# Optimization experiments

Hardware: AMD Instinct MI355X
Metric: run time of the kernel (lower is better)

## Reference

```python
import jax, jax.numpy as jnp
import numpy as np

L, C, H = 4, 512, 8
HD = C // H

def silu(x):
    return x * jax.nn.sigmoid(x)

def layernorm(x, g, b, eps=1e-5):
    m = x.mean(-1, keepdims=True)
    v = ((x - m) ** 2).mean(-1, keepdims=True)
    return (x - m) * jax.lax.rsqrt(v + eps) * g + b

def adaln(x, t, w, b):
    # x: (N,B,C), t: (B,C), w: (2C,C), b: (2C,)
    mod = silu(t) @ w.T + b
    scale, shift = jnp.split(mod, 2, axis=-1)
    return x * (1.0 + scale[None]) + shift[None]

def embed_rotary(x, pos):
    # x: (B,N,C), pos: (B,N,C,2) with [...,0]=cos, [...,1]=sin
    cos, sin = pos[..., 0], pos[..., 1]
    x2 = jnp.stack([-x[..., 1::2], x[..., 0::2]], axis=-1).reshape(x.shape)
    return x * cos + x2 * sin

def setup_inputs() -> dict:
    key = jax.random.key(0)
    ks = jax.random.split(key, 24)
    Nq, Nkv, B = 1024, 2048, 4
    query = jax.random.normal(ks[0], (Nq, B, C), jnp.float32)
    value = jax.random.normal(ks[1], (Nkv, B, C), jnp.float32)
    diff_ts = jax.random.normal(ks[2], (B, C), jnp.float32)
    # valid rotary codes: cos/sin of random angles
    aq = jax.random.uniform(ks[3], (B, Nq, C), jnp.float32, 0.0, 2 * np.pi)
    ak = jax.random.uniform(ks[4], (B, Nkv, C), jnp.float32, 0.0, 2 * np.pi)
    query_pos = jnp.stack([jnp.cos(aq), jnp.sin(aq)], axis=-1)
    value_pos = jnp.stack([jnp.cos(ak), jnp.sin(ak)], axis=-1)
    s = 0.02
    inp = dict(query=query, value=value, diff_ts=diff_ts,
               query_pos=query_pos, value_pos=value_pos,
               aw_attn=jax.random.normal(ks[5], (L, 2 * C, C)) * s,
               ab_attn=jax.random.normal(ks[6], (L, 2 * C)) * s,
               in_w=jax.random.normal(ks[7], (L, 3 * C, C)) * s,
               in_b=jnp.zeros((L, 3 * C)),
               out_w=jax.random.normal(ks[8], (L, C, C)) * s,
               out_b=jnp.zeros((L, C)),
               ln1_g=jnp.ones((L, C)), ln1_b=jnp.zeros((L, C)),
               aw_ffn=jax.random.normal(ks[9], (L, 2 * C, C)) * s,
               ab_ffn=jax.random.normal(ks[10], (L, 2 * C)) * s,
               w1=jax.random.normal(ks[11], (L, C, C)) * s,
               b1=jnp.zeros((L, C)),
               w2=jax.random.normal(ks[12], (L, C, C)) * s,
               b2=jnp.zeros((L, C)),
               ln2_g=jnp.ones((L, C)), ln2_b=jnp.zeros((L, C)))
    return inp

def _forward(query, value, diff_ts, query_pos, value_pos,
             aw_attn, ab_attn, in_w, in_b, out_w, out_b, ln1_g, ln1_b,
             aw_ffn, ab_ffn, w1, b1, w2, b2, ln2_g, ln2_b):
    Nq, B, _ = query.shape
    Nkv = value.shape[0]
    scaling = HD ** -0.5
    outputs = []
    q = query
    for i in range(L):
        # --- cross-attention layer ---
        aq = adaln(q, diff_ts, aw_attn[i], ab_attn[i])
        wq, wk, wv = jnp.split(in_w[i], 3, axis=0)
        bq, bk, bv = jnp.split(in_b[i], 3, axis=0)
        qp = (aq @ wq.T + bq) * scaling          # (Nq,B,C)
        kp = value @ wk.T + bk                    # (Nkv,B,C)
        vp = value @ wv.T + bv
        qb = embed_rotary(qp.transpose(1, 0, 2), query_pos)  # (B,Nq,C)
        kb = embed_rotary(kp.transpose(1, 0, 2), value_pos)  # (B,Nkv,C)
        vb = vp.transpose(1, 0, 2)
        qh = qb.reshape(B, Nq, H, HD).transpose(0, 2, 1, 3)   # (B,H,Nq,HD)
        kh = kb.reshape(B, Nkv, H, HD).transpose(0, 2, 1, 3)
        vh = vb.reshape(B, Nkv, H, HD).transpose(0, 2, 1, 3)
        scores = jnp.einsum('bhqd,bhkd->bhqk', qh, kh)
        attn = jax.nn.softmax(scores, axis=-1)
        o = jnp.einsum('bhqk,bhkd->bhqd', attn, vh)
        o = o.transpose(0, 2, 1, 3).reshape(B, Nq, C).transpose(1, 0, 2)  # (Nq,B,C)
        o = o @ out_w[i].T + out_b[i]
        q = layernorm(q + o, ln1_g[i], ln1_b[i])
        # --- feedforward layer (residual uses AdaLN-modulated x) ---
        xa = adaln(q, diff_ts, aw_ffn[i], ab_ffn[i])
        h = jax.nn.relu(xa @ w1[i].T + b1[i])
        h = h @ w2[i].T + b2[i]
        q = layernorm(xa + h, ln2_g[i], ln2_b[i])
        outputs.append(q)
    return jnp.stack(outputs)  # (L, Nq, B, C)

def reference(query, value, diff_ts, query_pos, value_pos,
              aw_attn, ab_attn, in_w, in_b, out_w, out_b, ln1_g, ln1_b,
              aw_ffn, ab_ffn, w1, b1, w2, b2, ln2_g, ln2_b):
    return _forward(query, value, diff_ts, query_pos, value_pos,
                    aw_attn, ab_attn, in_w, in_b, out_w, out_b, ln1_g, ln1_b,
                    aw_ffn, ab_ffn, w1, b1, w2, b2, ln2_g, ln2_b)
```

## Files before the change

kernel.cpp:

```cpp
#include <hip/hip_runtime.h>
#include <hip/hip_bf16.h>

typedef __hip_bfloat16 bf16;
typedef __attribute__((ext_vector_type(8))) short short8;
typedef __attribute__((ext_vector_type(4))) short s16x4;
typedef __attribute__((ext_vector_type(4))) float f32x4;

#define CDIM 512
#define BDIM 4
#define HDIM 8
#define HDQ  64
#define NQ   1024
#define NKV  2048
#define LAYERS 4
#define SPLIT 2

#if defined(__has_builtin)
#if __has_builtin(__builtin_amdgcn_global_load_lds)
#define USE_GLL 1
#endif
#endif

static __device__ __forceinline__ short f2s(float f) {
    bf16 h = __float2bfloat16(f);
    return *reinterpret_cast<short*>(&h);
}


__global__ __launch_bounds__(256) void convall_k(
    const float* __restrict__ s0, const float* __restrict__ s1,
    const float* __restrict__ s2, const float* __restrict__ s3,
    const float* __restrict__ s4,
    bf16* __restrict__ d0, bf16* __restrict__ d1, bf16* __restrict__ d2,
    bf16* __restrict__ d3, bf16* __restrict__ d4) {
    int gid = blockIdx.x * 256 + threadIdx.x;
    const float* src; bf16* dst; int off;
    if (gid < 1048576)      { src = s0; dst = d0; off = gid; }
    else if (gid < 1835008) { src = s1; dst = d1; off = gid - 1048576; }
    else if (gid < 2097152) { src = s2; dst = d2; off = gid - 1835008; }
    else if (gid < 2359296) { src = s3; dst = d3; off = gid - 2097152; }
    else                    { src = s4; dst = d4; off = gid - 2359296; }
    f32x4 v = *(const f32x4*)(src + (size_t)off * 4);
    s16x4 o;
    o[0] = f2s(v[0]); o[1] = f2s(v[1]); o[2] = f2s(v[2]); o[3] = f2s(v[3]);
    *(s16x4*)(dst + (size_t)off * 4) = o;
}

__global__ __launch_bounds__(256) void modall_k(const float* __restrict__ diff_ts,
    const float* __restrict__ aw_attn, const float* __restrict__ ab_attn,
    const float* __restrict__ aw_ffn,  const float* __restrict__ ab_ffn,
    float* __restrict__ mod) {
    int wv = blockIdx.x * 4 + (threadIdx.x >> 6);
    int lane = threadIdx.x & 63;
    int col  = wv & 1023;
    int b    = (wv >> 10) & 3;
    int kind = (wv >> 12) & 1;
    int l    = wv >> 13;
    const float* w = (kind ? aw_ffn : aw_attn) + ((size_t)l * 1024 + col) * CDIM + lane * 8;
    const float* tb = diff_ts + b * CDIM + lane * 8;
    f32x4 w0 = *(const f32x4*)w;
    f32x4 w1 = *(const f32x4*)(w + 4);
    f32x4 t0 = *(const f32x4*)tb;
    f32x4 t1 = *(const f32x4*)(tb + 4);
    #pragma unroll
    for (int j = 0; j < 4; ++j) {
        t0[j] = t0[j] / (1.f + __expf(-t0[j]));
        t1[j] = t1[j] / (1.f + __expf(-t1[j]));
    }
    f32x4 pp = w0 * t0 + w1 * t1;
    float acc = (pp[0] + pp[1]) + (pp[2] + pp[3]);
    #pragma unroll
    for (int off = 32; off; off >>= 1) acc += __shfl_xor(acc, off);
    if (lane == 0)
        mod[wv] = acc + (kind ? ab_ffn : ab_attn)[l * 1024 + col];
}

__global__ __launch_bounds__(256) void adaln_k(const float* __restrict__ x,
                                               const float* __restrict__ mod,
                                               bf16* __restrict__ outb) {
    int i = blockIdx.x * 256 + threadIdx.x;
    int c = i & 511;
    int b = (i >> 9) & 3;
    outb[i] = __float2bfloat16(x[i] * (1.f + mod[b * 1024 + c]) + mod[b * 1024 + 512 + c]);
}

__global__ __launch_bounds__(256) void ln_ad_k(const float* __restrict__ x,
                                               const float* __restrict__ res,
                                               const float* __restrict__ res2,
                                               const float* __restrict__ g,
                                               const float* __restrict__ bb,
                                               const float* __restrict__ mod,
                                               float* __restrict__ ln_f,
                                               float* __restrict__ ln_f2,
                                               float* __restrict__ ad_f,
                                               bf16* __restrict__ ad_b) {
    int row = blockIdx.x;
    int t = threadIdx.x;
    size_t base = (size_t)row * CDIM;
    float v0 = x[base + t] + res[base + t];
    float v1 = x[base + t + 256] + res[base + t + 256];
    if (res2) {
        v0 += res2[base + t];
        v1 += res2[base + t + 256];
    }
    float s1 = v0 + v1;
    float s2 = v0 * v0 + v1 * v1;
    #pragma unroll
    for (int off = 32; off; off >>= 1) {
        s1 += __shfl_xor(s1, off);
        s2 += __shfl_xor(s2, off);
    }
    __shared__ float a1[4], a2[4];
    int w = t >> 6;
    if ((t & 63) == 0) { a1[w] = s1; a2[w] = s2; }
    __syncthreads();
    s1 = a1[0] + a1[1] + a1[2] + a1[3];
    s2 = a2[0] + a2[1] + a2[2] + a2[3];
    float mean = s1 * (1.f / 512.f);
    float var = s2 * (1.f / 512.f) - mean * mean;
    float rs = rsqrtf(var + 1e-5f);
    float y0 = (v0 - mean) * rs * g[t] + bb[t];
    float y1 = (v1 - mean) * rs * g[t + 256] + bb[t + 256];
    if (ln_f)  { ln_f[base + t] = y0;  ln_f[base + t + 256] = y1; }
    if (ln_f2) { ln_f2[base + t] = y0; ln_f2[base + t + 256] = y1; }
    if (mod) {
        int b = row & 3;
        float o0 = y0 * (1.f + mod[b * 1024 + t]) + mod[b * 1024 + 512 + t];
        float o1 = y1 * (1.f + mod[b * 1024 + t + 256]) + mod[b * 1024 + 512 + t + 256];
        if (ad_f) { ad_f[base + t] = o0; ad_f[base + t + 256] = o1; }
        ad_b[base + t] = __float2bfloat16(o0);
        ad_b[base + t + 256] = __float2bfloat16(o1);
    }
}

template <int EPI, int WM, int NT, int KS, bool SWZ>
__global__ __launch_bounds__(256) void mgemm_k(
    const bf16* __restrict__ A, const bf16* __restrict__ Wt,
    const float* __restrict__ bias, void* __restrict__ out0v,
    void* __restrict__ out1v, int M, int N, int K,
    const float* __restrict__ pos, float scl, int Nseq) {
    __shared__ bf16 As[2][2][64 * 32];
    __shared__ bf16 Bs[2][2][64 * 32];
    int t = threadIdx.x;
    int w = t >> 6;
    int lane = t & 63;
    int l16 = lane & 15;
    int quad = lane >> 4;
    int wy = w >> 1, wx = w & 1;

    int bxi, byi, bzi;
    if (SWZ) {
        int nx = gridDim.x, ny = gridDim.y;
        int flat = (blockIdx.z * ny + blockIdx.y) * nx + blockIdx.x;
        int nwg = nx * ny * gridDim.z;
        int s = (flat & 7) * (nwg >> 3) + (flat >> 3);
        bxi = s % nx; int rest = s / nx; byi = rest % ny; bzi = rest / ny;
    } else {
        bxi = blockIdx.x; byi = blockIdx.y; bzi = blockIdx.z;
    }
    int bm = byi * 64;
    int bn = bxi * 64;

    int lr2 = lane >> 2;
    int lc4 = (lane & 3) ^ ((lane >> 3) & 3);

    int kbeg = 0, kend = K;
    if (KS == 2) { int half = K >> 1; kbeg = bzi * half; kend = kbeg + half; }

    f32x4 acc[WM][NT] = {};

    auto stage = [&](int buf, int k0) {
#if USE_GLL
        const bf16* sa = A + (size_t)(bm + w * 16 + lr2) * K + k0 + lc4 * 8;
        const bf16* sb = Wt + (size_t)(bn + w * 16 + lr2) * K + k0 + lc4 * 8;
        #pragma unroll
        for (int j = 0; j < 2; ++j) {
            __builtin_amdgcn_global_load_lds(
                (const unsigned int __attribute__((address_space(1)))*)(sa + j * 32),
                (unsigned int __attribute__((address_space(3)))*)(&As[buf][j][w * 512]),
                16, 0, 0);
            __builtin_amdgcn_global_load_lds(
                (const unsigned int __attribute__((address_space(1)))*)(sb + j * 32),
                (unsigned int __attribute__((address_space(3)))*)(&Bs[buf][j][w * 512]),
                16, 0, 0);
        }
#else
        for (int e = t; e < 512; e += 256) {
            int sub = e >> 8, c = e & 255;
            int row = c >> 2, c4 = c & 3;
            int srcc = c4 ^ ((row >> 1) & 3);
            *(uint4*)&As[buf][sub][row * 32 + c4 * 8] =
                *(const uint4*)(A + (size_t)(bm + row) * K + k0 + sub * 32 + srcc * 8);
            *(uint4*)&Bs[buf][sub][row * 32 + c4 * 8] =
                *(const uint4*)(Wt + (size_t)(bn + row) * K + k0 + sub * 32 + srcc * 8);
        }
#endif
    };

    stage(0, kbeg);
    __syncthreads();
    int cur = 0;
    int rchunk = (quad ^ ((l16 >> 1) & 3)) * 8;

    for (int k0 = kbeg; k0 < kend; k0 += 64) {
        if (k0 + 64 < kend) stage(cur ^ 1, k0 + 64);

        #pragma unroll
        for (int kk = 0; kk < 2; ++kk) {
            short8 af[WM], bfr[NT];
            #pragma unroll
            for (int mt = 0; mt < WM; ++mt)
                af[mt] = *(const short8*)
                    &As[cur][kk][((wy * WM + mt) * 16 + l16) * 32 + rchunk];
            #pragma unroll
            for (int nt = 0; nt < NT; ++nt)
                bfr[nt] = *(const short8*)
                    &Bs[cur][kk][((wx * NT + nt) * 16 + l16) * 32 + rchunk];
            #pragma unroll
            for (int mt = 0; mt < WM; ++mt)
                #pragma unroll
                for (int nt = 0; nt < NT; ++nt)
                    acc[mt][nt] = __builtin_amdgcn_mfma_f32_16x16x32_bf16(
                        af[mt], bfr[nt], acc[mt][nt], 0, 0, 0);
        }

        __syncthreads();
        cur ^= 1;
    }

    float* fout = (KS == 2 && bzi) ? (float*)out1v : (float*)out0v;
    #pragma unroll
    for (int nt = 0; nt < NT; ++nt) {
        int n = bn + (wx * NT + nt) * 16 + l16;
        float bnv = (EPI == 4 || (KS == 2 && bzi)) ? 0.f : bias[n];
        #pragma unroll
        for (int mt = 0; mt < WM; ++mt) {
            #pragma unroll
            for (int r = 0; r < 4; ++r) {
                int m = bm + (wy * WM + mt) * 16 + quad * 4 + r;
                float v = acc[mt][nt][r] + ((EPI == 4) ? bias[m] : bnv);
                if (EPI == 0) {
                    fout[(size_t)m * N + n] = v;
                } else if (EPI == 1) {
                    ((bf16*)out0v)[(size_t)m * N + n] = __float2bfloat16(fmaxf(v, 0.f));
                } else if (EPI == 4) {
                    int hh = m >> 6, dd = m & 63;
                    int bsel = n & 3, key = n >> 2;
                    ((bf16*)out0v)[((size_t)(bsel * HDIM + hh) * HDQ + dd) * NKV + key] =
                        __float2bfloat16(v);
                } else {
                    v *= scl;
                    int c = n;
                    int nseq = m >> 2, b = m & 3;
                    float part = __shfl_xor(v, 1);
                    const float* pp = pos + (((size_t)b * Nseq + nseq) * CDIM + c) * 2;
                    float cs = pp[0], sn = pp[1];
                    float o = (l16 & 1) ? (v * cs + part * sn) : (v * cs - part * sn);
                    bf16* op = (bf16*)out0v +
                               ((size_t)(b * HDIM + (c >> 6)) * Nseq + nseq) * HDQ + (c & 63);
                    *op = __float2bfloat16(o);
                }
            }
        }
    }
}

__global__ __launch_bounds__(256) void attn4_k(const bf16* __restrict__ qh,
                                               const bf16* __restrict__ kh,
                                               const bf16* __restrict__ vT,
                                               float* __restrict__ pl,
                                               float* __restrict__ pacc) {
    __shared__ short Kb[2][64 * 64];
    __shared__ short Vb[2][64 * 64];
    __shared__ short Ps[4][16 * 64];
    int t = threadIdx.x;
    int wave = t >> 6, lane = t & 63;
    int l16 = lane & 15, quad = lane >> 4;

    int b0 = blockIdx.x;
    int newid = (b0 & 7) * 128 + (b0 >> 3);
    int qtile = newid & 15;
    int grp = newid >> 4;
    int split = grp & 1;
    int bh = grp >> 1;
    int q0 = qtile * 64 + wave * 16;
    int kbase = split * (NKV / SPLIT);

    const bf16* qbase = qh + ((size_t)bh * NQ + q0) * HDQ;
    short8 aq0 = *(const short8*)(qbase + (size_t)l16 * HDQ + quad * 8);
    short8 aq1 = *(const short8*)(qbase + (size_t)l16 * HDQ + 32 + quad * 8);
    const bf16* kbh = kh + ((size_t)bh * NKV + kbase) * HDQ;
    const bf16* vbh = vT + (size_t)bh * HDQ * NKV + kbase;

    int r0 = wave * 16;
    int lr = lane >> 3;
    int swz_src = ((lane & 7) ^ lr) * 8;

    auto stage = [&](int buf, int kt) {
#if USE_GLL
        #pragma unroll
        for (int j = 0; j < 2; ++j) {
            int rr = r0 + j * 8;
            __builtin_amdgcn_global_load_lds(
                (const unsigned int __attribute__((address_space(1)))*)
                    (kbh + (size_t)(kt + rr + lr) * HDQ + swz_src),
                (unsigned int __attribute__((address_space(3)))*)&Kb[buf][rr * 64],
                16, 0, 0);
            __builtin_amdgcn_global_load_lds(
                (const unsigned int __attribute__((address_space(1)))*)
                    (vbh + (size_t)(rr + lr) * NKV + kt + swz_src),
                (unsigned int __attribute__((address_space(3)))*)&Vb[buf][rr * 64],
                16, 0, 0);
        }
#else
        #pragma unroll
        for (int j = 0; j < 2; ++j) {
            int rr = r0 + j * 8 + lr;
            int lc = lane & 7;
            *(short8*)&Kb[buf][rr * 64 + ((lc ^ (rr & 7)) * 8)] =
                *(const short8*)(kbh + (size_t)(kt + rr) * HDQ + lc * 8);
            *(short8*)&Vb[buf][rr * 64 + ((lc ^ (rr & 7)) * 8)] =
                *(const short8*)(vbh + (size_t)rr * NKV + kt + lc * 8);
        }
#endif
    };

    f32x4 accO[4] = {};
    float lsum[4] = {0.f, 0.f, 0.f, 0.f};

    stage(0, 0);
    __syncthreads();
    int cur = 0;
    int swz_m = l16 & 7;

    for (int kt = 0; kt < NKV / SPLIT; kt += 64) {
        if (kt + 64 < NKV / SPLIT) stage(cur ^ 1, kt + 64);

        f32x4 sc[4] = {};
        #pragma unroll
        for (int nt = 0; nt < 4; ++nt) {
            const short* kr = &Kb[cur][(nt * 16 + l16) * 64];
            short8 bk0 = *(const short8*)&kr[(quad ^ swz_m) * 8];
            short8 bk1 = *(const short8*)&kr[((quad + 4) ^ swz_m) * 8];
            sc[nt] = __builtin_amdgcn_mfma_f32_16x16x32_bf16(aq0, bk0, sc[nt], 0, 0, 0);
            sc[nt] = __builtin_amdgcn_mfma_f32_16x16x32_bf16(aq1, bk1, sc[nt], 0, 0, 0);
        }

        #pragma unroll
        for (int r = 0; r < 4; ++r) {
            float p0 = exp2f(sc[0][r]);
            float p1 = exp2f(sc[1][r]);
            float p2 = exp2f(sc[2][r]);
            float p3 = exp2f(sc[3][r]);
            lsum[r] += (p0 + p1) + (p2 + p3);
            int pr = quad * 4 + r;
            short* prow = &Ps[wave][pr * 64];
            int pm = pr & 7;
            int ch = l16 >> 3, kl = l16 & 7;
            prow[((ch ^ pm) << 3) + kl]       = f2s(p0);
            prow[(((ch + 2) ^ pm) << 3) + kl] = f2s(p1);
            prow[(((ch + 4) ^ pm) << 3) + kl] = f2s(p2);
            prow[(((ch + 6) ^ pm) << 3) + kl] = f2s(p3);
        }

        const short* prd = &Ps[wave][l16 * 64];
        short8 pa0 = *(const short8*)&prd[(quad ^ swz_m) * 8];
        short8 pa1 = *(const short8*)&prd[((quad + 4) ^ swz_m) * 8];
        #pragma unroll
        for (int nt = 0; nt < 4; ++nt) {
            const short* vr = &Vb[cur][(nt * 16 + l16) * 64];
            short8 bv0 = *(const short8*)&vr[(quad ^ swz_m) * 8];
            short8 bv1 = *(const short8*)&vr[((quad + 4) ^ swz_m) * 8];
            accO[nt] = __builtin_amdgcn_mfma_f32_16x16x32_bf16(pa0, bv0, accO[nt], 0, 0, 0);
            accO[nt] = __builtin_amdgcn_mfma_f32_16x16x32_bf16(pa1, bv1, accO[nt], 0, 0, 0);
        }

        __syncthreads();
        cur ^= 1;
    }

    #pragma unroll
    for (int r = 0; r < 4; ++r) {
        #pragma unroll
        for (int off = 1; off < 16; off <<= 1) lsum[r] += __shfl_xor(lsum[r], off);
    }

    size_t rowbase = ((size_t)split * 32 + bh) * NQ + q0;
    #pragma unroll
    for (int r = 0; r < 4; ++r) {
        size_t row = rowbase + quad * 4 + r;
        if (l16 == 0) pl[row] = lsum[r];
        #pragma unroll
        for (int nt = 0; nt < 4; ++nt)
            pacc[row * 64 + nt * 16 + l16] = accO[nt][r];
    }
}

__global__ __launch_bounds__(256) void attn_comb_k(const float* __restrict__ pl,
                                                   const float* __restrict__ pacc,
                                                   bf16* __restrict__ o) {
    int idx = blockIdx.x * 256 + threadIdx.x;
    int d = idx & 63;
    int row = idx >> 6;
    int q = row & (NQ - 1);
    int bh = row >> 10;
    const int S = 32 * NQ;
    float l = pl[row] + pl[S + row];
    float v = pacc[(size_t)row * 64 + d] + pacc[(size_t)(S + row) * 64 + d];
    int b = bh >> 3, h = bh & 7;
    o[((size_t)(q * BDIM + b)) * CDIM + h * HDQ + d] = __float2bfloat16(v / l);
}


extern "C" void kernel_launch(void* const* d_in, const int* in_sizes, int n_in,
                              void* d_out, int out_size, void* d_ws, size_t ws_size,
                              hipStream_t stream) {
    const float* query     = (const float*)d_in[0];
    const float* value     = (const float*)d_in[1];
    const float* diff_ts   = (const float*)d_in[2];
    const float* query_pos = (const float*)d_in[3];
    const float* value_pos = (const float*)d_in[4];
    const float* aw_attn   = (const float*)d_in[5];
    const float* ab_attn   = (const float*)d_in[6];
    const float* in_w      = (const float*)d_in[7];
    const float* in_b      = (const float*)d_in[8];
    const float* out_w     = (const float*)d_in[9];
    const float* out_b     = (const float*)d_in[10];
    const float* ln1_g     = (const float*)d_in[11];
    const float* ln1_b     = (const float*)d_in[12];
    const float* aw_ffn    = (const float*)d_in[13];
    const float* ab_ffn    = (const float*)d_in[14];
    const float* w1        = (const float*)d_in[15];
    const float* b1        = (const float*)d_in[16];
    const float* w2        = (const float*)d_in[17];
    const float* b2        = (const float*)d_in[18];
    const float* ln2_g     = (const float*)d_in[19];
    const float* ln2_b     = (const float*)d_in[20];
    float* out_f = (float*)d_out;

    float* ws      = (float*)d_ws;
    float* mod_ws  = ws + 2048;
    float* q_cur   = ws + 34816;
    float* buf_a   = q_cur + 2097152;
    float* buf_p   = buf_a + 2097152;
    bf16* a_bf     = (bf16*)(buf_p + 2097152);
    bf16* h_bf     = a_bf + 2097152;
    bf16* qh       = h_bf + 2097152;
    bf16* kh       = qh + 2097152;
    bf16* vt       = kh + 4194304;
    bf16* val_bf   = vt + 4194304;
    bf16* winb     = val_bf + 4194304;
    bf16* woutb    = winb + 3145728;
    bf16* w1b      = woutb + 1048576;
    bf16* w2b      = w1b + 1048576;
    float* buf_p2  = (float*)(w2b + 1048576);
    float* pacc    = buf_a;
    float* pl      = (float*)a_bf;

    const int MQ = NQ * BDIM;
    const int MKV = NKV * BDIM;
    const float scaling = 0.125f * 1.44269504f;

    modall_k<<<8192, 256, 0, stream>>>(diff_ts, aw_attn, ab_attn, aw_ffn, ab_ffn, mod_ws);
    convall_k<<<10240, 256, 0, stream>>>(value, in_w, out_w, w1, w2,
                                         val_bf, winb, woutb, w1b, w2b);
    adaln_k<<<(MQ * CDIM) / 256, 256, 0, stream>>>(query, mod_ws, a_bf);

    for (int i = 0; i < LAYERS; ++i) {
        const float* mod_ffn  = mod_ws + i * 8192 + 4096;
        const float* mod_attn_next = (i + 1 < LAYERS) ? (mod_ws + (i + 1) * 8192) : nullptr;
        const bf16* winb_i = winb + (size_t)i * 1536 * CDIM;
        const float* in_b_i = in_b + (size_t)i * 1536;
        const float* qsrc = (i == 0) ? query : q_cur;

        mgemm_k<2, 2, 2, 1, true><<<dim3(8, MQ / 64), 256, 0, stream>>>(
            a_bf, winb_i, in_b_i, qh, nullptr, MQ, 512, CDIM, query_pos, scaling, NQ);
        mgemm_k<2, 2, 2, 1, true><<<dim3(8, MKV / 64), 256, 0, stream>>>(
            val_bf, winb_i + (size_t)512 * CDIM, in_b_i + 512, kh, nullptr, MKV, 512,
            CDIM, value_pos, 1.f, NKV);
        mgemm_k<4, 2, 2, 1, false><<<dim3(MKV / 64, 8), 256, 0, stream>>>(
            winb_i + (size_t)1024 * CDIM, val_bf, in_b_i + 1024, vt, nullptr,
            512, MKV, CDIM, nullptr, 0.f, 0);
        attn4_k<<<1024, 256, 0, stream>>>(qh, kh, vt, pl, pacc);
        attn_comb_k<<<8192, 256, 0, stream>>>(pl, pacc, h_bf);
        mgemm_k<0, 2, 2, 2, true><<<dim3(8, MQ / 64, 2), 256, 0, stream>>>(
            h_bf, woutb + (size_t)i * CDIM * CDIM, out_b + i * CDIM, buf_p, buf_p2,
            MQ, 512, CDIM, nullptr, 0.f, 0);
        ln_ad_k<<<MQ, 256, 0, stream>>>(qsrc, buf_p, buf_p2,
                                        ln1_g + i * CDIM, ln1_b + i * CDIM,
                                        mod_ffn, nullptr, nullptr, buf_a, a_bf);
        mgemm_k<1, 2, 2, 1, true><<<dim3(8, MQ / 64), 256, 0, stream>>>(
            a_bf, w1b + (size_t)i * CDIM * CDIM, b1 + i * CDIM, h_bf, nullptr,
            MQ, 512, CDIM, nullptr, 0.f, 0);
        mgemm_k<0, 2, 2, 2, true><<<dim3(8, MQ / 64, 2), 256, 0, stream>>>(
            h_bf, w2b + (size_t)i * CDIM * CDIM, b2 + i * CDIM, buf_p, buf_p2,
            MQ, 512, CDIM, nullptr, 0.f, 0);
        ln_ad_k<<<MQ, 256, 0, stream>>>(buf_a, buf_p, buf_p2,
                                        ln2_g + i * CDIM, ln2_b + i * CDIM,
                                        mod_attn_next, q_cur,
                                        out_f + (size_t)i * MQ * CDIM, nullptr, a_bf);
    }
}
```

Before: 709.3 us.

## Fuse K and V projections into one kernel and read K/V directly from global in attention

Replaces the two separate K-projection and transposed V-projection GEMMs with a single kernel that shares the staged value tile across both weight matrices, then applies rotary to K and writes V transposed in the epilogue. The attention kernel drops its LDS double-buffered K/V staging and barriers, loading MFMA operands straight from global memory (relying on cache), and uses a padded P buffer instead of XOR swizzle. The goal is to halve reads of the value activations and cut synchronisation. The costs are uncoalesced transposed V stores, more global traffic per wave in attention, and possible LDS bank conflicts from the padding.

```diff
diff --git a/kernel.cpp b/kernel.cpp
--- a/kernel.cpp
+++ b/kernel.cpp
@@ -232,22 +232,17 @@
     #pragma unroll
     for (int nt = 0; nt < NT; ++nt) {
         int n = bn + (wx * NT + nt) * 16 + l16;
-        float bnv = (EPI == 4 || (KS == 2 && bzi)) ? 0.f : bias[n];
+        float bnv = (KS == 2 && bzi) ? 0.f : bias[n];
         #pragma unroll
         for (int mt = 0; mt < WM; ++mt) {
             #pragma unroll
             for (int r = 0; r < 4; ++r) {
                 int m = bm + (wy * WM + mt) * 16 + quad * 4 + r;
-                float v = acc[mt][nt][r] + ((EPI == 4) ? bias[m] : bnv);
+                float v = acc[mt][nt][r] + bnv;
                 if (EPI == 0) {
                     fout[(size_t)m * N + n] = v;
                 } else if (EPI == 1) {
                     ((bf16*)out0v)[(size_t)m * N + n] = __float2bfloat16(fmaxf(v, 0.f));
-                } else if (EPI == 4) {
-                    int hh = m >> 6, dd = m & 63;
-                    int bsel = n & 3, key = n >> 2;
-                    ((bf16*)out0v)[((size_t)(bsel * HDIM + hh) * HDQ + dd) * NKV + key] =
-                        __float2bfloat16(v);
                 } else {
                     v *= scl;
                     int c = n;
@@ -265,14 +260,138 @@
     }
 }
 
-__global__ __launch_bounds__(256) void attn4_k(const bf16* __restrict__ qh,
+__global__ __launch_bounds__(256) void kv_k(
+    const bf16* __restrict__ val, const bf16* __restrict__ Wk,
+    const bf16* __restrict__ Wv, const float* __restrict__ biask,
+    const float* __restrict__ biasv, bf16* __restrict__ kh,
+    bf16* __restrict__ vt, const float* __restrict__ vpos) {
+    __shared__ bf16 As[2][2][64 * 32];
+    __shared__ bf16 Bk[2][2][64 * 32];
+    __shared__ bf16 Bv[2][2][64 * 32];
+    int t = threadIdx.x;
+    int w = t >> 6;
+    int lane = t & 63;
+    int l16 = lane & 15;
+    int quad = lane >> 4;
+    int wy = w >> 1, wx = w & 1;
+
+    int flat = blockIdx.x;
+    int s = (flat & 7) * 128 + (flat >> 3);
+    int bn = (s & 7) * 64;
+    int bm = (s >> 3) * 64;
+    const int K = CDIM;
+
+    int lr2 = lane >> 2;
+    int lc4 = (lane & 3) ^ ((lane >> 3) & 3);
+
+    f32x4 acck[2][2] = {};
+    f32x4 accv[2][2] = {};
+
+    auto stage = [&](int buf, int k0) {
+#if USE_GLL
+        const bf16* sa = val + (size_t)(bm + w * 16 + lr2) * K + k0 + lc4 * 8;
+        const bf16* sk = Wk + (size_t)(bn + w * 16 + lr2) * K + k0 + lc4 * 8;
+        const bf16* sv = Wv + (size_t)(bn + w * 16 + lr2) * K + k0 + lc4 * 8;
+        #pragma unroll
+        for (int j = 0; j < 2; ++j) {
+            __builtin_amdgcn_global_load_lds(
+                (const unsigned int __attribute__((address_space(1)))*)(sa + j * 32),
+                (unsigned int __attribute__((address_space(3)))*)(&As[buf][j][w * 512]),
+                16, 0, 0);
+            __builtin_amdgcn_global_load_lds(
+                (const unsigned int __attribute__((address_space(1)))*)(sk + j * 32),
+                (unsigned int __attribute__((address_space(3)))*)(&Bk[buf][j][w * 512]),
+                16, 0, 0);
+            __builtin_amdgcn_global_load_lds(
+                (const unsigned int __attribute__((address_space(1)))*)(sv + j * 32),
+                (unsigned int __attribute__((address_space(3)))*)(&Bv[buf][j][w * 512]),
+                16, 0, 0);
+        }
+#else
+        for (int e = t; e < 512; e += 256) {
+            int sub = e >> 8, c = e & 255;
+            int row = c >> 2, c4 = c & 3;
+            int srcc = c4 ^ ((row >> 1) & 3);
+            *(uint4*)&As[buf][sub][row * 32 + c4 * 8] =
+                *(const uint4*)(val + (size_t)(bm + row) * K + k0 + sub * 32 + srcc * 8);
+            *(uint4*)&Bk[buf][sub][row * 32 + c4 * 8] =
+                *(const uint4*)(Wk + (size_t)(bn + row) * K + k0 + sub * 32 + srcc * 8);
+            *(uint4*)&Bv[buf][sub][row * 32 + c4 * 8] =
+                *(const uint4*)(Wv + (size_t)(bn + row) * K + k0 + sub * 32 + srcc * 8);
+        }
+#endif
+    };
+
+    stage(0, 0);
+    __syncthreads();
+    int cur = 0;
+    int rchunk = (quad ^ ((l16 >> 1) & 3)) * 8;
+
+    for (int k0 = 0; k0 < K; k0 += 64) {
+        if (k0 + 64 < K) stage(cur ^ 1, k0 + 64);
+
+        #pragma unroll
+        for (int kk = 0; kk < 2; ++kk) {
+            short8 af[2], bkf[2], bvf[2];
+            #pragma unroll
+            for (int mt = 0; mt < 2; ++mt)
+                af[mt] = *(const short8*)
+                    &As[cur][kk][((wy * 2 + mt) * 16 + l16) * 32 + rchunk];
+            #pragma unroll
+            for (int nt = 0; nt < 2; ++nt) {
+                bkf[nt] = *(const short8*)
+                    &Bk[cur][kk][((wx * 2 + nt) * 16 + l16) * 32 + rchunk];
+                bvf[nt] = *(const short8*)
+                    &Bv[cur][kk][((wx * 2 + nt) * 16 + l16) * 32 + rchunk];
+            }
+            #pragma unroll
+            for (int mt = 0; mt < 2; ++mt)
+                #pragma unroll
+                for (int nt = 0; nt < 2; ++nt) {
+                    acck[mt][nt] = __builtin_amdgcn_mfma_f32_16x16x32_bf16(
+                        af[mt], bkf[nt], acck[mt][nt], 0, 0, 0);
+                    accv[mt][nt] = __builtin_amdgcn_mfma_f32_16x16x32_bf16(
+                        af[mt], bvf[nt], accv[mt][nt], 0, 0, 0);
+                }
+        }
+
+        __syncthreads();
+        cur ^= 1;
+    }
+
+    #pragma unroll
+    for (int nt = 0; nt < 2; ++nt) {
+        int n = bn + (wx * 2 + nt) * 16 + l16;
+        float bk_n = biask[n];
+        float bv_n = biasv[n];
+        int d = n & 63, hh = n >> 6;
+        #pragma unroll
+        for (int mt = 0; mt < 2; ++mt) {
+            #pragma unroll
+            for (int r = 0; r < 4; ++r) {
+                int m = bm + (wy * 2 + mt) * 16 + quad * 4 + r;
+                int nseq = m >> 2, b = m & 3;
+                float v = acck[mt][nt][r] + bk_n;
+                float part = __shfl_xor(v, 1);
+                const float* pp = vpos + (((size_t)b * NKV + nseq) * CDIM + n) * 2;
+                float cs = pp[0], sn = pp[1];
+                float o = (l16 & 1) ? (v * cs + part * sn) : (v * cs - part * sn);
+                kh[((size_t)(b * HDIM + (n >> 6)) * NKV + nseq) * HDQ + (n & 63)] =
+                    __float2bfloat16(o);
+                float vv = accv[mt][nt][r] + bv_n;
+                vt[((size_t)(b * HDIM + hh) * HDQ + d) * NKV + nseq] =
+                    __float2bfloat16(vv);
+            }
+        }
+    }
+}
+
+__global__ __launch_bounds__(256) void attn5_k(const bf16* __restrict__ qh,
                                                const bf16* __restrict__ kh,
                                                const bf16* __restrict__ vT,
                                                float* __restrict__ pl,
                                                float* __restrict__ pacc) {
-    __shared__ short Kb[2][64 * 64];
-    __shared__ short Vb[2][64 * 64];
-    __shared__ short Ps[4][16 * 64];
+    __shared__ short Ps[4][16 * 72];
     int t = threadIdx.x;
     int wave = t >> 6, lane = t & 63;
     int l16 = lane & 15, quad = lane >> 4;
@@ -292,56 +411,17 @@
     const bf16* kbh = kh + ((size_t)bh * NKV + kbase) * HDQ;
     const bf16* vbh = vT + (size_t)bh * HDQ * NKV + kbase;
 
-    int r0 = wave * 16;
-    int lr = lane >> 3;
-    int swz_src = ((lane & 7) ^ lr) * 8;
-
-    auto stage = [&](int buf, int kt) {
-#if USE_GLL
-        #pragma unroll
-        for (int j = 0; j < 2; ++j) {
-            int rr = r0 + j * 8;
-            __builtin_amdgcn_global_load_lds(
-                (const unsigned int __attribute__((address_space(1)))*)
-                    (kbh + (size_t)(kt + rr + lr) * HDQ + swz_src),
-                (unsigned int __attribute__((address_space(3)))*)&Kb[buf][rr * 64],
-                16, 0, 0);
-            __builtin_amdgcn_global_load_lds(
-                (const unsigned int __attribute__((address_space(1)))*)
-                    (vbh + (size_t)(rr + lr) * NKV + kt + swz_src),
-                (unsigned int __attribute__((address_space(3)))*)&Vb[buf][rr * 64],
-                16, 0, 0);
-        }
-#else
-        #pragma unroll
-        for (int j = 0; j < 2; ++j) {
-            int rr = r0 + j * 8 + lr;
-            int lc = lane & 7;
-            *(short8*)&Kb[buf][rr * 64 + ((lc ^ (rr & 7)) * 8)] =
-                *(const short8*)(kbh + (size_t)(kt + rr) * HDQ + lc * 8);
-            *(short8*)&Vb[buf][rr * 64 + ((lc ^ (rr & 7)) * 8)] =
-                *(const short8*)(vbh + (size_t)rr * NKV + kt + lc * 8);
-        }
-#endif
-    };
-
     f32x4 accO[4] = {};
     float lsum[4] = {0.f, 0.f, 0.f, 0.f};
-
-    stage(0, 0);
-    __syncthreads();
-    int cur = 0;
-    int swz_m = l16 & 7;
+    short* myPs = Ps[wave];
 
     for (int kt = 0; kt < NKV / SPLIT; kt += 64) {
-        if (kt + 64 < NKV / SPLIT) stage(cur ^ 1, kt + 64);
-
         f32x4 sc[4] = {};
         #pragma unroll
         for (int nt = 0; nt < 4; ++nt) {
-            const short* kr = &Kb[cur][(nt * 16 + l16) * 64];
-            short8 bk0 = *(const short8*)&kr[(quad ^ swz_m) * 8];
-            short8 bk1 = *(const short8*)&kr[((quad + 4) ^ swz_m) * 8];
+            const bf16* kr = kbh + (size_t)(kt + nt * 16 + l16) * HDQ;
+            short8 bk0 = *(const short8*)(kr + quad * 8);
+            short8 bk1 = *(const short8*)(kr + 32 + quad * 8);
             sc[nt] = __builtin_amdgcn_mfma_f32_16x16x32_bf16(aq0, bk0, sc[nt], 0, 0, 0);
             sc[nt] = __builtin_amdgcn_mfma_f32_16x16x32_bf16(aq1, bk1, sc[nt], 0, 0, 0);
         }
@@ -354,29 +434,24 @@
             float p3 = exp2f(sc[3][r]);
             lsum[r] += (p0 + p1) + (p2 + p3);
             int pr = quad * 4 + r;
-            short* prow = &Ps[wave][pr * 64];
-            int pm = pr & 7;
-            int ch = l16 >> 3, kl = l16 & 7;
-            prow[((ch ^ pm) << 3) + kl]       = f2s(p0);
-            prow[(((ch + 2) ^ pm) << 3) + kl] = f2s(p1);
-            prow[(((ch + 4) ^ pm) << 3) + kl] = f2s(p2);
-            prow[(((ch + 6) ^ pm) << 3) + kl] = f2s(p3);
-        }
-
-        const short* prd = &Ps[wave][l16 * 64];
-        short8 pa0 = *(const short8*)&prd[(quad ^ swz_m) * 8];
-        short8 pa1 = *(const short8*)&prd[((quad + 4) ^ swz_m) * 8];
+            short* prow = &myPs[pr * 72];
+            prow[l16]      = f2s(p0);
+            prow[16 + l16] = f2s(p1);
+            prow[32 + l16] = f2s(p2);
+            prow[48 + l16] = f2s(p3);
+        }
+
+        const short* prd = &myPs[l16 * 72];
+        short8 pa0 = *(const short8*)&prd[quad * 8];
+        short8 pa1 = *(const short8*)&prd[32 + quad * 8];
         #pragma unroll
         for (int nt = 0; nt < 4; ++nt) {
-            const short* vr = &Vb[cur][(nt * 16 + l16) * 64];
-            short8 bv0 = *(const short8*)&vr[(quad ^ swz_m) * 8];
-            short8 bv1 = *(const short8*)&vr[((quad + 4) ^ swz_m) * 8];
+            const bf16* vr = vbh + (size_t)(nt * 16 + l16) * NKV + kt;
+            short8 bv0 = *(const short8*)(vr + quad * 8);
+            short8 bv1 = *(const short8*)(vr + 32 + quad * 8);
             accO[nt] = __builtin_amdgcn_mfma_f32_16x16x32_bf16(pa0, bv0, accO[nt], 0, 0, 0);
             accO[nt] = __builtin_amdgcn_mfma_f32_16x16x32_bf16(pa1, bv1, accO[nt], 0, 0, 0);
         }
-
-        __syncthreads();
-        cur ^= 1;
     }
 
     #pragma unroll
@@ -458,7 +533,6 @@
     float* pl      = (float*)a_bf;
 
     const int MQ = NQ * BDIM;
-    const int MKV = NKV * BDIM;
     const float scaling = 0.125f * 1.44269504f;
 
     modall_k<<<8192, 256, 0, stream>>>(diff_ts, aw_attn, ab_attn, aw_ffn, ab_ffn, mod_ws);
@@ -475,13 +549,10 @@
 
         mgemm_k<2, 2, 2, 1, true><<<dim3(8, MQ / 64), 256, 0, stream>>>(
             a_bf, winb_i, in_b_i, qh, nullptr, MQ, 512, CDIM, query_pos, scaling, NQ);
-        mgemm_k<2, 2, 2, 1, true><<<dim3(8, MKV / 64), 256, 0, stream>>>(
-            val_bf, winb_i + (size_t)512 * CDIM, in_b_i + 512, kh, nullptr, MKV, 512,
-            CDIM, value_pos, 1.f, NKV);
-        mgemm_k<4, 2, 2, 1, false><<<dim3(MKV / 64, 8), 256, 0, stream>>>(
-            winb_i + (size_t)1024 * CDIM, val_bf, in_b_i + 1024, vt, nullptr,
-            512, MKV, CDIM, nullptr, 0.f, 0);
-        attn4_k<<<1024, 256, 0, stream>>>(qh, kh, vt, pl, pacc);
+        kv_k<<<1024, 256, 0, stream>>>(
+            val_bf, winb_i + (size_t)512 * CDIM, winb_i + (size_t)1024 * CDIM,
+            in_b_i + 512, in_b_i + 1024, kh, vt, value_pos);
+        attn5_k<<<1024, 256, 0, stream>>>(qh, kh, vt, pl, pacc);
         attn_comb_k<<<8192, 256, 0, stream>>>(pl, pacc, h_bf);
         mgemm_k<0, 2, 2, 2, true><<<dim3(8, MQ / 64, 2), 256, 0, stream>>>(
             h_bf, woutb + (size_t)i * CDIM * CDIM, out_b + i * CDIM, buf_p, buf_p2,
```

New measurement: 1.017 ms. +43.4%, slower.
